# Optimization experiments

Hardware: AMD Instinct MI355X
Metric: run time of the kernel (lower is better)

Reference implementation:

```python
import jax, jax.numpy as jnp
import numpy as np

NUM_GROUPS = 16
EPS = 1e-6


def setup_inputs() -> dict:
    key = jax.random.key(0)
    ks = jax.random.split(key, 6)
    b, c, t, h, w = 2, 256, 4, 32, 32
    x = jax.random.normal(ks[0], (b, c, t, h, w), dtype=jnp.float32)
    scale = 0.02
    return {
        "x": x,
        "gamma": jnp.ones((c,), jnp.float32),
        "beta": jnp.zeros((c,), jnp.float32),
        "wq": jax.random.normal(ks[1], (c, c), jnp.float32) * scale,
        "bq": jnp.zeros((c,), jnp.float32),
        "wk": jax.random.normal(ks[2], (c, c), jnp.float32) * scale,
        "bk": jnp.zeros((c,), jnp.float32),
        "wv": jax.random.normal(ks[3], (c, c), jnp.float32) * scale,
        "bv": jnp.zeros((c,), jnp.float32),
        "wp": jax.random.normal(ks[4], (c, c), jnp.float32) * scale,
        "bp": jnp.zeros((c,), jnp.float32),
    }


def _group_norm(x, gamma, beta):
    b, c, t, h, w = x.shape
    xg = x.reshape(b, NUM_GROUPS, -1)  # [b, G, (c/G)*t*h*w]
    mu = jnp.mean(xg, axis=2, keepdims=True)
    var = jnp.var(xg, axis=2, keepdims=True)
    xn = ((xg - mu) * jax.lax.rsqrt(var + EPS)).reshape(b, c, t, h, w)
    return xn * gamma[None, :, None, None, None] + beta[None, :, None, None, None]


def reference(x, gamma, beta, wq, bq, wk, bk, wv, bv, wp, bp):
    b, c, t, h, w = x.shape
    n = t * h * w
    hn = _group_norm(x, gamma, beta).reshape(b, c, n)  # [b, c, n]
    # 1x1x1 conv == channel matmul
    q = jnp.einsum("oc,bcn->bon", wq, hn) + bq[None, :, None]
    k = jnp.einsum("oc,bcn->bon", wk, hn) + bk[None, :, None]
    v = jnp.einsum("oc,bcn->bon", wv, hn) + bv[None, :, None]
    # scores[b, i, j] = sum_c q[b,c,i] k[b,c,j] / sqrt(c)
    scores = jnp.einsum("bci,bcj->bij", q, k) * (float(c) ** -0.5)
    attn = jax.nn.softmax(scores, axis=2)  # [b, n, n]
    # h_[b, c, i] = sum_j v[b,c,j] attn[b,i,j]
    ho = jnp.einsum("bcj,bij->bci", v, attn)
    out = jnp.einsum("oc,bcn->bon", wp, ho) + bp[None, :, None]
    return x + out.reshape(b, c, t, h, w)
```

## Files before the change

kernel.cpp:

```cpp
#include <hip/hip_runtime.h>
#include <hip/hip_bf16.h>

#define NB 2
#define NC 256
#define NN 4096
#define NG 16
#define GSZ (16*NN)
#define SPLIT 4
#define JT (NN / SPLIT / 64)
#define SCL 0.09014205f
#define THRRAW 88.0f

typedef __attribute__((ext_vector_type(8))) short bf16x8;
typedef __attribute__((ext_vector_type(4))) float f32x4;
typedef __attribute__((ext_vector_type(8))) unsigned short u16x8;

static __device__ __forceinline__ unsigned short f2b(float f) {
    union { float f; unsigned u; } x; x.f = f;
    unsigned r = x.u + 0x7fffu + ((x.u >> 16) & 1u);
    return (unsigned short)(r >> 16);
}
static __device__ __forceinline__ float b2f(unsigned short u) {
    union { unsigned u; float f; } x; x.u = ((unsigned)u) << 16;
    return x.f;
}
static __device__ __forceinline__ void glds16(const void* g, void* l) {
    __builtin_amdgcn_global_load_lds(
        (const __attribute__((address_space(1))) unsigned int*)g,
        (__attribute__((address_space(3))) unsigned int*)l, 16, 0, 0);
}

__global__ void k_wcvt(const float* __restrict__ wq, const float* __restrict__ wk,
                       const float* __restrict__ wv, const float* __restrict__ wp,
                       unsigned short* __restrict__ dst) {
    int idx = (blockIdx.x * 256 + threadIdx.x) * 4;
    int which = idx >> 16, off = idx & 65535;
    const float* s = (which == 0) ? wq : (which == 1) ? wk : (which == 2) ? wv : wp;
    float4 v = *(const float4*)(s + off);
    dst[idx + 0] = f2b(v.x);
    dst[idx + 1] = f2b(v.y);
    dst[idx + 2] = f2b(v.z);
    dst[idx + 3] = f2b(v.w);
}

__global__ void k_stats(const float* __restrict__ x, float* __restrict__ stats) {
    int bg = blockIdx.x >> 3, seg = blockIdx.x & 7;
    const float4* p = (const float4*)(x + (size_t)bg * GSZ + (size_t)seg * (GSZ / 8));
    float s1 = 0.f, s2 = 0.f;
    for (int k = threadIdx.x; k < GSZ / 8 / 4; k += 256) {
        float4 v = p[k];
        s1 += v.x + v.y + v.z + v.w;
        s2 += v.x*v.x + v.y*v.y + v.z*v.z + v.w*v.w;
    }
    #pragma unroll
    for (int m = 1; m < 64; m <<= 1) { s1 += __shfl_xor(s1, m); s2 += __shfl_xor(s2, m); }
    __shared__ float r1[4], r2[4];
    int w = threadIdx.x >> 6;
    if ((threadIdx.x & 63) == 0) { r1[w] = s1; r2[w] = s2; }
    __syncthreads();
    if (threadIdx.x == 0) {
        float a = 0.f, b = 0.f;
        #pragma unroll
        for (int i = 0; i < 4; i++) { a += r1[i]; b += r2[i]; }
        atomicAdd(&stats[bg * 2], a);
        atomicAdd(&stats[bg * 2 + 1], b);
    }
}

__global__ void k_norm_t(const float* __restrict__ x, const float* __restrict__ gamma,
                         const float* __restrict__ beta, const float* __restrict__ stats,
                         unsigned short* __restrict__ hn_t) {
    __shared__ unsigned short tile[64][66];
    int n0 = blockIdx.x * 64, c0 = blockIdx.y * 64, b = blockIdx.z;
    int cc = threadIdx.x >> 2, part = threadIdx.x & 3;
    int c = c0 + cc;
    float s1 = stats[(b * NG + (c >> 4)) * 2];
    float s2 = stats[(b * NG + (c >> 4)) * 2 + 1];
    float mean = s1 * (1.f / (float)GSZ);
    float var  = s2 * (1.f / (float)GSZ) - mean * mean;
    float rstd = rsqrtf(var + 1e-6f);
    float sc = rstd * gamma[c];
    float sh = beta[c] - mean * sc;
    const float4* row = (const float4*)(x + ((size_t)b * NC + c) * NN + n0);
    #pragma unroll
    for (int q = 0; q < 4; q++) {
        int f4 = part * 4 + q;
        float4 v = row[f4];
        tile[cc][f4*4+0] = f2b(v.x * sc + sh);
        tile[cc][f4*4+1] = f2b(v.y * sc + sh);
        tile[cc][f4*4+2] = f2b(v.z * sc + sh);
        tile[cc][f4*4+3] = f2b(v.w * sc + sh);
    }
    __syncthreads();
    int nn = threadIdx.x >> 2;
    u16x8 o0, o1;
    #pragma unroll
    for (int e = 0; e < 8; e++) { o0[e] = tile[part*16 + e][nn]; o1[e] = tile[part*16 + 8 + e][nn]; }
    unsigned short* dst = hn_t + ((size_t)b * NN + n0 + nn) * NC + c0 + part * 16;
    *(u16x8*)dst = o0;
    *(u16x8*)(dst + 8) = o1;
}

__global__ __launch_bounds__(256, 2) void k_qkv(
        const unsigned short* __restrict__ hn_t, const unsigned short* __restrict__ wb,
        const float* __restrict__ bq, const float* __restrict__ bk, const float* __restrict__ bv,
        unsigned short* __restrict__ q_t, unsigned short* __restrict__ k_t,
        unsigned short* __restrict__ v_cm) {
    int i0 = blockIdx.x * 64, which = blockIdx.y, b = blockIdx.z;
    int lane = threadIdx.x & 63, w = threadIdx.x >> 6;
    const unsigned short* W = wb + which * 65536;
    const float* bias = (which == 0) ? bq : (which == 1) ? bk : bv;
    if (which < 2) {
        const unsigned short* arow =
            hn_t + ((size_t)b * NN + i0 + w * 16 + (lane & 15)) * NC + ((lane >> 4) * 8);
        f32x4 acc[16];
        #pragma unroll
        for (int t = 0; t < 16; t++) acc[t] = (f32x4){0.f, 0.f, 0.f, 0.f};
        #pragma unroll
        for (int kk = 0; kk < 8; kk++) {
            bf16x8 af = *(const bf16x8*)(arow + kk * 32);
            const unsigned short* bbase = W + (size_t)(lane & 15) * NC + kk * 32 + ((lane >> 4) * 8);
            #pragma unroll
            for (int ot = 0; ot < 16; ot++) {
                bf16x8 bf_ = *(const bf16x8*)(bbase + (size_t)ot * 16 * NC);
                acc[ot] = __builtin_amdgcn_mfma_f32_16x16x32_bf16(af, bf_, acc[ot], 0, 0, 0);
            }
        }
        unsigned short* dst = ((which == 0) ? q_t : k_t) + (size_t)b * NN * NC;
        #pragma unroll
        for (int ot = 0; ot < 16; ot++) {
            float bv_ = bias[ot * 16 + (lane & 15)];
            #pragma unroll
            for (int r = 0; r < 4; r++) {
                int i = i0 + w * 16 + (lane >> 4) * 4 + r;
                dst[(size_t)i * NC + ot * 16 + (lane & 15)] = f2b(acc[ot][r] + bv_);
            }
        }
    } else {
        f32x4 acc[4][4];
        #pragma unroll
        for (int mt = 0; mt < 4; mt++)
            #pragma unroll
            for (int nt = 0; nt < 4; nt++) acc[mt][nt] = (f32x4){0.f, 0.f, 0.f, 0.f};
        #pragma unroll
        for (int kk = 0; kk < 8; kk++) {
            bf16x8 bfr[4];
            #pragma unroll
            for (int nt = 0; nt < 4; nt++)
                bfr[nt] = *(const bf16x8*)(hn_t + ((size_t)b * NN + i0 + nt * 16 + (lane & 15)) * NC
                                           + kk * 32 + ((lane >> 4) * 8));
            #pragma unroll
            for (int mt = 0; mt < 4; mt++) {
                bf16x8 af = *(const bf16x8*)(W + (size_t)(w * 64 + mt * 16 + (lane & 15)) * NC
                                             + kk * 32 + ((lane >> 4) * 8));
                #pragma unroll
                for (int nt = 0; nt < 4; nt++)
                    acc[mt][nt] = __builtin_amdgcn_mfma_f32_16x16x32_bf16(af, bfr[nt], acc[mt][nt], 0, 0, 0);
            }
        }
        #pragma unroll
        for (int mt = 0; mt < 4; mt++) {
            #pragma unroll
            for (int r = 0; r < 4; r++) {
                int o = w * 64 + mt * 16 + (lane >> 4) * 4 + r;
                float bv_ = bias[o];
                #pragma unroll
                for (int nt = 0; nt < 4; nt++) {
                    int i = i0 + nt * 16 + (lane & 15);
                    v_cm[(size_t)b * NC * NN + (size_t)o * NN + i] = f2b(acc[mt][nt][r] + bv_);
                }
            }
        }
    }
}

__global__ __launch_bounds__(512, 2) void k_attn(
        const unsigned short* __restrict__ q_t, const unsigned short* __restrict__ k_t,
        const unsigned short* __restrict__ v_cm,
        unsigned short* __restrict__ po, float* __restrict__ ml) {
    __shared__ __attribute__((aligned(16))) unsigned short Ks[2][16384];
    __shared__ __attribute__((aligned(16))) unsigned short Vs[2][16384];
    __shared__ __attribute__((aligned(16))) unsigned short Ps[8][1024];
    int bid = blockIdx.x;
    int g = bid & 7, xb = bid >> 3;
    int sp = g & 3, b = g >> 2;
    int i0 = xb * 128;
    int lane = threadIdx.x & 63, w = threadIdx.x >> 6;
    size_t bO = (size_t)b * NN * NC;
    bf16x8 qf[8];
    {
        const unsigned short* qrow =
            q_t + bO + (size_t)(i0 + w * 16 + (lane & 15)) * NC + ((lane >> 4) * 8);
        #pragma unroll
        for (int kk = 0; kk < 8; kk++) qf[kk] = *(const bf16x8*)(qrow + kk * 32);
    }
    unsigned kstat[4], vstat[4];
    #pragma unroll
    for (int r = 0; r < 4; r++) {
        int jr = r * 16 + w * 2 + (lane >> 5);
        kstat[r] = (unsigned)(jr * 512 + (((lane & 31) * 16) ^ ((jr & 7) << 4)));
        int cr = r * 64 + w * 8 + (lane >> 3);
        vstat[r] = (unsigned)(cr * 8192 + (((lane & 7) * 16) ^ ((cr & 7) << 4)));
    }
    const char* kp = (const char*)(k_t + bO) + (size_t)sp * 524288;
    const char* vp = (const char*)(v_cm + bO) + (size_t)sp * 2048;
    f32x4 o[16];
    #pragma unroll
    for (int t = 0; t < 16; t++) o[t] = (f32x4){0.f, 0.f, 0.f, 0.f};
    float m = -1e30f, l = 0.f;
    #pragma unroll
    for (int r = 0; r < 4; r++) {
        glds16(kp + kstat[r], (char*)&Ks[0][0] + w * 1024 + r * 8192);
        glds16(vp + vstat[r], (char*)&Vs[0][0] + w * 1024 + r * 8192);
    }
    __syncthreads();
    int cur = 0;
    #pragma unroll 1
    for (int t = 0; t < JT; ++t) {
        if (t < JT - 1) {
            kp += 32768; vp += 128;
            int nb = cur ^ 1;
            #pragma unroll
            for (int r = 0; r < 4; r++) {
                glds16(kp + kstat[r], (char*)&Ks[nb][0] + w * 1024 + r * 8192);
                glds16(vp + vstat[r], (char*)&Vs[nb][0] + w * 1024 + r * 8192);
            }
        }
        const char* KsB = (const char*)&Ks[cur][0];
        const char* VsB = (const char*)&Vs[cur][0];
        f32x4 s[4];
        #pragma unroll
        for (int tt = 0; tt < 4; tt++) s[tt] = (f32x4){0.f, 0.f, 0.f, 0.f};
        __builtin_amdgcn_s_setprio(1);
        #pragma unroll
        for (int kk = 0; kk < 8; kk++) {
            #pragma unroll
            for (int tt = 0; tt < 4; tt++) {
                unsigned off = ((unsigned)((tt * 16 + (lane & 15)) * 512 + kk * 64 + ((lane >> 4) * 16)))
                               ^ (((unsigned)(lane & 7)) << 4);
                bf16x8 kf = *(const bf16x8*)(KsB + off);
                s[tt] = __builtin_amdgcn_mfma_f32_16x16x32_bf16(kf, qf[kk], s[tt], 0, 0, 0);
            }
        }
        __builtin_amdgcn_s_setprio(0);
        float lm = -1e30f;
        #pragma unroll
        for (int tt = 0; tt < 4; tt++)
            #pragma unroll
            for (int r = 0; r < 4; r++) lm = fmaxf(lm, s[tt][r]);
        lm = fmaxf(lm, __shfl_xor(lm, 16));
        lm = fmaxf(lm, __shfl_xor(lm, 32));
        float tmax = lm - m;
        tmax = fmaxf(tmax, __shfl_xor(tmax, 1));
        tmax = fmaxf(tmax, __shfl_xor(tmax, 2));
        tmax = fmaxf(tmax, __shfl_xor(tmax, 4));
        tmax = fmaxf(tmax, __shfl_xor(tmax, 8));
        if (tmax > THRRAW) {
            float mn = fmaxf(m, lm);
            float corr = exp2f((m - mn) * SCL);
            m = mn;
            l *= corr;
            #pragma unroll
            for (int r = 0; r < 4; r++) {
                float cr_ = __shfl(corr, (lane & 48) | ((lane >> 4) * 4 + r));
                #pragma unroll
                for (int ct = 0; ct < 16; ct++) o[ct][r] *= cr_;
            }
        }
        float rs = 0.f;
        #pragma unroll
        for (int tt = 0; tt < 4; tt++) {
            unsigned long long pw = 0ull;
            #pragma unroll
            for (int r = 0; r < 4; r++) {
                float p = exp2f((s[tt][r] - m) * SCL);
                rs += p;
                pw |= (unsigned long long)f2b(p) << (r * 16);
            }
            unsigned off = ((unsigned)((lane & 15) * 128 + tt * 32 + ((lane >> 4) * 8)))
                           ^ (((unsigned)(lane & 7)) << 4);
            *(unsigned long long*)((char*)&Ps[w][0] + off) = pw;
        }
        rs += __shfl_xor(rs, 16);
        rs += __shfl_xor(rs, 32);
        l += rs;
        __builtin_amdgcn_s_setprio(1);
        #pragma unroll
        for (int kk = 0; kk < 2; kk++) {
            unsigned offp = ((unsigned)((lane & 15) * 128 + kk * 64 + ((lane >> 4) * 16)))
                            ^ (((unsigned)(lane & 7)) << 4);
            bf16x8 pf = *(const bf16x8*)((char*)&Ps[w][0] + offp);
            #pragma unroll
            for (int ct = 0; ct < 16; ct++) {
                unsigned offv = ((unsigned)((ct * 16 + (lane & 15)) * 128 + kk * 64 + ((lane >> 4) * 16)))
                                ^ (((unsigned)(lane & 7)) << 4);
                bf16x8 vf = *(const bf16x8*)(VsB + offv);
                o[ct] = __builtin_amdgcn_mfma_f32_16x16x32_bf16(pf, vf, o[ct], 0, 0, 0);
            }
        }
        __builtin_amdgcn_s_setprio(0);
        __syncthreads();
        cur ^= 1;
    }
    unsigned short* dst = po + (size_t)(sp * NB + b) * NN * NC;
    #pragma unroll
    for (int ct = 0; ct < 16; ct++) {
        #pragma unroll
        for (int r = 0; r < 4; r++) {
            int i = i0 + w * 16 + (lane >> 4) * 4 + r;
            dst[(size_t)i * NC + ct * 16 + (lane & 15)] = f2b(o[ct][r]);
        }
    }
    if (lane < 16) {
        int i = i0 + w * 16 + lane;
        size_t mi = ((size_t)(sp * NB + b) * NN + i) * 2;
        ml[mi] = m;
        ml[mi + 1] = l;
    }
}

__global__ __launch_bounds__(256, 4) void k_proj(
        const unsigned short* __restrict__ po, const float* __restrict__ ml,
        const unsigned short* __restrict__ wp_b, const float* __restrict__ bp,
        const float* __restrict__ x, float* __restrict__ out) {
    __shared__ __attribute__((aligned(16))) unsigned short Hs[32 * 256];
    int i0 = blockIdx.x * 32, b = blockIdx.y;
    int tid = threadIdx.x, lane = tid & 63, w = tid >> 6;
    {
        int il = tid >> 3, cq = tid & 7;
        int i = i0 + il;
        float mv[SPLIT], lv[SPLIT];
        float M = -1e30f;
        #pragma unroll
        for (int s = 0; s < SPLIT; s++) {
            size_t mi = ((size_t)(s * NB + b) * NN + i) * 2;
            mv[s] = ml[mi]; lv[s] = ml[mi + 1];
            M = fmaxf(M, mv[s]);
        }
        float den = 0.f, wg[SPLIT];
        #pragma unroll
        for (int s = 0; s < SPLIT; s++) { wg[s] = exp2f((mv[s] - M) * SCL); den += wg[s] * lv[s]; }
        float inv = 1.f / den;
        #pragma unroll
        for (int s = 0; s < SPLIT; s++) wg[s] *= inv;
        #pragma unroll
        for (int e = 0; e < 4; e++) {
            float accv[8];
            #pragma unroll
            for (int q = 0; q < 8; q++) accv[q] = 0.f;
            #pragma unroll
            for (int s = 0; s < SPLIT; s++) {
                u16x8 v = *(const u16x8*)(po + ((size_t)(s * NB + b) * NN + i) * NC + cq * 32 + e * 8);
                #pragma unroll
                for (int q = 0; q < 8; q++) accv[q] += wg[s] * b2f(v[q]);
            }
            u16x8 rv;
            #pragma unroll
            for (int q = 0; q < 8; q++) rv[q] = f2b(accv[q]);
            unsigned off = ((unsigned)(il * 512 + cq * 64 + e * 16)) ^ ((il & 7) << 4);
            *(u16x8*)((char*)Hs + off) = rv;
        }
    }
    __syncthreads();
    f32x4 acc[4][2];
    #pragma unroll
    for (int mt = 0; mt < 4; mt++)
        #pragma unroll
        for (int nt = 0; nt < 2; nt++) acc[mt][nt] = (f32x4){0.f, 0.f, 0.f, 0.f};
    #pragma unroll
    for (int kk = 0; kk < 8; kk++) {
        bf16x8 bfr[2];
        #pragma unroll
        for (int nt = 0; nt < 2; nt++) {
            unsigned off = ((unsigned)((nt * 16 + (lane & 15)) * 512 + kk * 64 + ((lane >> 4) * 16)))
                           ^ (((unsigned)(lane & 7)) << 4);
            bfr[nt] = *(const bf16x8*)((char*)Hs + off);
        }
        #pragma unroll
        for (int mt = 0; mt < 4; mt++) {
            bf16x8 af = *(const bf16x8*)(wp_b + (size_t)(w * 64 + mt * 16 + (lane & 15)) * NC
                                         + kk * 32 + ((lane >> 4) * 8));
            #pragma unroll
            for (int nt = 0; nt < 2; nt++)
                acc[mt][nt] = __builtin_amdgcn_mfma_f32_16x16x32_bf16(af, bfr[nt], acc[mt][nt], 0, 0, 0);
        }
    }
    #pragma unroll
    for (int mt = 0; mt < 4; mt++) {
        #pragma unroll
        for (int r = 0; r < 4; r++) {
            int o = w * 64 + mt * 16 + (lane >> 4) * 4 + r;
            float bv_ = bp[o];
            #pragma unroll
            for (int nt = 0; nt < 2; nt++) {
                int i = i0 + nt * 16 + (lane & 15);
                size_t idx = ((size_t)b * NC + o) * NN + i;
                out[idx] = x[idx] + acc[mt][nt][r] + bv_;
            }
        }
    }
}

extern "C" void kernel_launch(void* const* d_in, const int* in_sizes, int n_in,
                              void* d_out, int out_size, void* d_ws, size_t ws_size,
                              hipStream_t stream) {
    const float* x     = (const float*)d_in[0];
    const float* gamma = (const float*)d_in[1];
    const float* beta  = (const float*)d_in[2];
    const float* wq    = (const float*)d_in[3];
    const float* bq    = (const float*)d_in[4];
    const float* wk    = (const float*)d_in[5];
    const float* bk    = (const float*)d_in[6];
    const float* wv    = (const float*)d_in[7];
    const float* bv    = (const float*)d_in[8];
    const float* wp    = (const float*)d_in[9];
    const float* bp    = (const float*)d_in[10];
    float* out = (float*)d_out;

    char* ws = (char*)d_ws;
    const size_t MB = 1024 * 1024;
    float*          stats = (float*)ws;
    unsigned short* wb    = (unsigned short*)(ws + 1024);
    unsigned short* q_t   = (unsigned short*)(ws + 1 * MB);
    unsigned short* k_t   = (unsigned short*)(ws + 5 * MB);
    unsigned short* v_cm  = (unsigned short*)(ws + 9 * MB);
    float*          ml    = (float*)(ws + 13 * MB);
    unsigned short* hn_t  = (unsigned short*)(ws + 14 * MB);
    unsigned short* po    = (unsigned short*)(ws + 14 * MB);

    hipMemsetAsync(stats, 0, 1024, stream);
    k_wcvt<<<256, 256, 0, stream>>>(wq, wk, wv, wp, wb);
    k_stats<<<256, 256, 0, stream>>>(x, stats);
    k_norm_t<<<dim3(NN / 64, NC / 64, NB), 256, 0, stream>>>(x, gamma, beta, stats, hn_t);
    k_qkv<<<dim3(NN / 64, 3, NB), 256, 0, stream>>>(hn_t, wb, bq, bk, bv, q_t, k_t, v_cm);
    k_attn<<<256, 512, 0, stream>>>(q_t, k_t, v_cm, po, ml);
    k_proj<<<dim3(NN / 32, NB), 256, 0, stream>>>(po, ml, wb + 3 * 65536, bp, x, out);
}
```

Measured before the change: 203.3 us.

## Fuse group-norm apply into QKV projection and merge stats with weight conversion

Weight conversion and group-norm statistics now run in one launch, selected by block index. The normalize-and-transpose kernel is removed. Each QKV block normalizes a 32-column slice of x into swizzled LDS, then computes Q, K and V from it. This drops two launches and the round trip of the bf16 hn_t buffer through global memory, at the cost of smaller per-block tiles and weight reads repeated across more blocks.

```diff
diff --git a/kernel.cpp b/kernel.cpp
--- a/kernel.cpp
+++ b/kernel.cpp
@@ -30,131 +30,142 @@
         (__attribute__((address_space(3))) unsigned int*)l, 16, 0, 0);
 }
 
-__global__ void k_wcvt(const float* __restrict__ wq, const float* __restrict__ wk,
-                       const float* __restrict__ wv, const float* __restrict__ wp,
-                       unsigned short* __restrict__ dst) {
-    int idx = (blockIdx.x * 256 + threadIdx.x) * 4;
-    int which = idx >> 16, off = idx & 65535;
-    const float* s = (which == 0) ? wq : (which == 1) ? wk : (which == 2) ? wv : wp;
-    float4 v = *(const float4*)(s + off);
-    dst[idx + 0] = f2b(v.x);
-    dst[idx + 1] = f2b(v.y);
-    dst[idx + 2] = f2b(v.z);
-    dst[idx + 3] = f2b(v.w);
-}
-
-__global__ void k_stats(const float* __restrict__ x, float* __restrict__ stats) {
-    int bg = blockIdx.x >> 3, seg = blockIdx.x & 7;
-    const float4* p = (const float4*)(x + (size_t)bg * GSZ + (size_t)seg * (GSZ / 8));
-    float s1 = 0.f, s2 = 0.f;
-    for (int k = threadIdx.x; k < GSZ / 8 / 4; k += 256) {
-        float4 v = p[k];
-        s1 += v.x + v.y + v.z + v.w;
-        s2 += v.x*v.x + v.y*v.y + v.z*v.z + v.w*v.w;
-    }
-    #pragma unroll
-    for (int m = 1; m < 64; m <<= 1) { s1 += __shfl_xor(s1, m); s2 += __shfl_xor(s2, m); }
+__global__ void k_pre(const float* __restrict__ wq, const float* __restrict__ wk,
+                      const float* __restrict__ wv, const float* __restrict__ wp,
+                      unsigned short* __restrict__ wbd,
+                      const float* __restrict__ x, float* __restrict__ stats) {
     __shared__ float r1[4], r2[4];
-    int w = threadIdx.x >> 6;
-    if ((threadIdx.x & 63) == 0) { r1[w] = s1; r2[w] = s2; }
-    __syncthreads();
-    if (threadIdx.x == 0) {
-        float a = 0.f, b = 0.f;
-        #pragma unroll
-        for (int i = 0; i < 4; i++) { a += r1[i]; b += r2[i]; }
-        atomicAdd(&stats[bg * 2], a);
-        atomicAdd(&stats[bg * 2 + 1], b);
-    }
-}
-
-__global__ void k_norm_t(const float* __restrict__ x, const float* __restrict__ gamma,
-                         const float* __restrict__ beta, const float* __restrict__ stats,
-                         unsigned short* __restrict__ hn_t) {
-    __shared__ unsigned short tile[64][66];
-    int n0 = blockIdx.x * 64, c0 = blockIdx.y * 64, b = blockIdx.z;
-    int cc = threadIdx.x >> 2, part = threadIdx.x & 3;
-    int c = c0 + cc;
-    float s1 = stats[(b * NG + (c >> 4)) * 2];
-    float s2 = stats[(b * NG + (c >> 4)) * 2 + 1];
-    float mean = s1 * (1.f / (float)GSZ);
-    float var  = s2 * (1.f / (float)GSZ) - mean * mean;
-    float rstd = rsqrtf(var + 1e-6f);
-    float sc = rstd * gamma[c];
-    float sh = beta[c] - mean * sc;
-    const float4* row = (const float4*)(x + ((size_t)b * NC + c) * NN + n0);
-    #pragma unroll
-    for (int q = 0; q < 4; q++) {
-        int f4 = part * 4 + q;
-        float4 v = row[f4];
-        tile[cc][f4*4+0] = f2b(v.x * sc + sh);
-        tile[cc][f4*4+1] = f2b(v.y * sc + sh);
-        tile[cc][f4*4+2] = f2b(v.z * sc + sh);
-        tile[cc][f4*4+3] = f2b(v.w * sc + sh);
-    }
-    __syncthreads();
-    int nn = threadIdx.x >> 2;
-    u16x8 o0, o1;
-    #pragma unroll
-    for (int e = 0; e < 8; e++) { o0[e] = tile[part*16 + e][nn]; o1[e] = tile[part*16 + 8 + e][nn]; }
-    unsigned short* dst = hn_t + ((size_t)b * NN + n0 + nn) * NC + c0 + part * 16;
-    *(u16x8*)dst = o0;
-    *(u16x8*)(dst + 8) = o1;
-}
-
-__global__ __launch_bounds__(256, 2) void k_qkv(
-        const unsigned short* __restrict__ hn_t, const unsigned short* __restrict__ wb,
+    int bx = blockIdx.x;
+    if (bx < 256) {
+        int bg = bx >> 3, seg = bx & 7;
+        const float4* p = (const float4*)(x + (size_t)bg * GSZ + (size_t)seg * (GSZ / 8));
+        float s1 = 0.f, s2 = 0.f;
+        for (int k = threadIdx.x; k < GSZ / 8 / 4; k += 256) {
+            float4 v = p[k];
+            s1 += v.x + v.y + v.z + v.w;
+            s2 += v.x*v.x + v.y*v.y + v.z*v.z + v.w*v.w;
+        }
+        #pragma unroll
+        for (int m = 1; m < 64; m <<= 1) { s1 += __shfl_xor(s1, m); s2 += __shfl_xor(s2, m); }
+        int w = threadIdx.x >> 6;
+        if ((threadIdx.x & 63) == 0) { r1[w] = s1; r2[w] = s2; }
+        __syncthreads();
+        if (threadIdx.x == 0) {
+            float a = 0.f, b = 0.f;
+            #pragma unroll
+            for (int i = 0; i < 4; i++) { a += r1[i]; b += r2[i]; }
+            atomicAdd(&stats[bg * 2], a);
+            atomicAdd(&stats[bg * 2 + 1], b);
+        }
+    } else {
+        int idx = ((bx - 256) * 256 + threadIdx.x) * 4;
+        int which = idx >> 16, off = idx & 65535;
+        const float* s = (which == 0) ? wq : (which == 1) ? wk : (which == 2) ? wv : wp;
+        float4 v = *(const float4*)(s + off);
+        wbd[idx + 0] = f2b(v.x);
+        wbd[idx + 1] = f2b(v.y);
+        wbd[idx + 2] = f2b(v.z);
+        wbd[idx + 3] = f2b(v.w);
+    }
+}
+
+__global__ __launch_bounds__(256, 2) void k_qkvn(
+        const float* __restrict__ x, const float* __restrict__ gamma,
+        const float* __restrict__ beta, const float* __restrict__ stats,
+        const unsigned short* __restrict__ wb,
         const float* __restrict__ bq, const float* __restrict__ bk, const float* __restrict__ bv,
         unsigned short* __restrict__ q_t, unsigned short* __restrict__ k_t,
         unsigned short* __restrict__ v_cm) {
-    int i0 = blockIdx.x * 64, which = blockIdx.y, b = blockIdx.z;
-    int lane = threadIdx.x & 63, w = threadIdx.x >> 6;
-    const unsigned short* W = wb + which * 65536;
-    const float* bias = (which == 0) ? bq : (which == 1) ? bk : bv;
-    if (which < 2) {
-        const unsigned short* arow =
-            hn_t + ((size_t)b * NN + i0 + w * 16 + (lane & 15)) * NC + ((lane >> 4) * 8);
-        f32x4 acc[16];
-        #pragma unroll
-        for (int t = 0; t < 16; t++) acc[t] = (f32x4){0.f, 0.f, 0.f, 0.f};
+    __shared__ __attribute__((aligned(16))) unsigned short hs[32 * 256];
+    int i0 = blockIdx.x * 32, b = blockIdx.y;
+    int tid = threadIdx.x, lane = tid & 63, w = tid >> 6;
+    {
+        int c = tid;
+        float s1 = stats[(b * NG + (c >> 4)) * 2];
+        float s2 = stats[(b * NG + (c >> 4)) * 2 + 1];
+        float mean = s1 * (1.f / (float)GSZ);
+        float var  = s2 * (1.f / (float)GSZ) - mean * mean;
+        float rstd = rsqrtf(var + 1e-6f);
+        float sc = rstd * gamma[c];
+        float sh = beta[c] - mean * sc;
+        const float4* row = (const float4*)(x + ((size_t)b * NC + c) * NN + i0);
+        #pragma unroll
+        for (int q = 0; q < 8; q++) {
+            float4 v = row[q];
+            float vals[4] = {v.x, v.y, v.z, v.w};
+            #pragma unroll
+            for (int e = 0; e < 4; e++) {
+                int i = q * 4 + e;
+                unsigned off = (unsigned)(i * 512 + ((c * 2) ^ ((i & 7) << 4)));
+                *(unsigned short*)((char*)hs + off) = f2b(vals[e] * sc + sh);
+            }
+        }
+    }
+    __syncthreads();
+    #pragma unroll 1
+    for (int which = 0; which < 2; ++which) {
+        const unsigned short* W = wb + which * 65536;
+        const float* bias = (which == 0) ? bq : bk;
+        unsigned short* dst = ((which == 0) ? q_t : k_t) + (size_t)b * NN * NC;
+        f32x4 acc[2][4];
+        #pragma unroll
+        for (int it = 0; it < 2; it++)
+            #pragma unroll
+            for (int ot = 0; ot < 4; ot++) acc[it][ot] = (f32x4){0.f, 0.f, 0.f, 0.f};
         #pragma unroll
         for (int kk = 0; kk < 8; kk++) {
-            bf16x8 af = *(const bf16x8*)(arow + kk * 32);
-            const unsigned short* bbase = W + (size_t)(lane & 15) * NC + kk * 32 + ((lane >> 4) * 8);
-            #pragma unroll
-            for (int ot = 0; ot < 16; ot++) {
-                bf16x8 bf_ = *(const bf16x8*)(bbase + (size_t)ot * 16 * NC);
-                acc[ot] = __builtin_amdgcn_mfma_f32_16x16x32_bf16(af, bf_, acc[ot], 0, 0, 0);
-            }
-        }
-        unsigned short* dst = ((which == 0) ? q_t : k_t) + (size_t)b * NN * NC;
-        #pragma unroll
-        for (int ot = 0; ot < 16; ot++) {
-            float bv_ = bias[ot * 16 + (lane & 15)];
-            #pragma unroll
-            for (int r = 0; r < 4; r++) {
-                int i = i0 + w * 16 + (lane >> 4) * 4 + r;
-                dst[(size_t)i * NC + ot * 16 + (lane & 15)] = f2b(acc[ot][r] + bv_);
-            }
-        }
-    } else {
-        f32x4 acc[4][4];
+            bf16x8 af[2];
+            #pragma unroll
+            for (int it = 0; it < 2; it++) {
+                unsigned row = (unsigned)(it * 16 + (lane & 15));
+                unsigned off = row * 512 + (((unsigned)(kk * 64 + ((lane >> 4) * 16))) ^ ((row & 7) << 4));
+                af[it] = *(const bf16x8*)((char*)hs + off);
+            }
+            #pragma unroll
+            for (int ot = 0; ot < 4; ot++) {
+                bf16x8 bf_ = *(const bf16x8*)(W + (size_t)(w * 64 + ot * 16 + (lane & 15)) * NC
+                                              + kk * 32 + ((lane >> 4) * 8));
+                #pragma unroll
+                for (int it = 0; it < 2; it++)
+                    acc[it][ot] = __builtin_amdgcn_mfma_f32_16x16x32_bf16(af[it], bf_, acc[it][ot], 0, 0, 0);
+            }
+        }
+        #pragma unroll
+        for (int it = 0; it < 2; it++) {
+            #pragma unroll
+            for (int ot = 0; ot < 4; ot++) {
+                int o = w * 64 + ot * 16 + (lane & 15);
+                float bv_ = bias[o];
+                #pragma unroll
+                for (int r = 0; r < 4; r++) {
+                    int i = i0 + it * 16 + (lane >> 4) * 4 + r;
+                    dst[(size_t)i * NC + o] = f2b(acc[it][ot][r] + bv_);
+                }
+            }
+        }
+    }
+    {
+        const unsigned short* W = wb + 2 * 65536;
+        f32x4 acc[4][2];
         #pragma unroll
         for (int mt = 0; mt < 4; mt++)
             #pragma unroll
-            for (int nt = 0; nt < 4; nt++) acc[mt][nt] = (f32x4){0.f, 0.f, 0.f, 0.f};
+            for (int nt = 0; nt < 2; nt++) acc[mt][nt] = (f32x4){0.f, 0.f, 0.f, 0.f};
         #pragma unroll
         for (int kk = 0; kk < 8; kk++) {
-            bf16x8 bfr[4];
-            #pragma unroll
-            for (int nt = 0; nt < 4; nt++)
-                bfr[nt] = *(const bf16x8*)(hn_t + ((size_t)b * NN + i0 + nt * 16 + (lane & 15)) * NC
-                                           + kk * 32 + ((lane >> 4) * 8));
+            bf16x8 bfr[2];
+            #pragma unroll
+            for (int nt = 0; nt < 2; nt++) {
+                unsigned row = (unsigned)(nt * 16 + (lane & 15));
+                unsigned off = row * 512 + (((unsigned)(kk * 64 + ((lane >> 4) * 16))) ^ ((row & 7) << 4));
+                bfr[nt] = *(const bf16x8*)((char*)hs + off);
+            }
             #pragma unroll
             for (int mt = 0; mt < 4; mt++) {
                 bf16x8 af = *(const bf16x8*)(W + (size_t)(w * 64 + mt * 16 + (lane & 15)) * NC
                                              + kk * 32 + ((lane >> 4) * 8));
                 #pragma unroll
-                for (int nt = 0; nt < 4; nt++)
+                for (int nt = 0; nt < 2; nt++)
                     acc[mt][nt] = __builtin_amdgcn_mfma_f32_16x16x32_bf16(af, bfr[nt], acc[mt][nt], 0, 0, 0);
             }
         }
@@ -163,9 +174,9 @@
             #pragma unroll
             for (int r = 0; r < 4; r++) {
                 int o = w * 64 + mt * 16 + (lane >> 4) * 4 + r;
-                float bv_ = bias[o];
-                #pragma unroll
-                for (int nt = 0; nt < 4; nt++) {
+                float bv_ = bv[o];
+                #pragma unroll
+                for (int nt = 0; nt < 2; nt++) {
                     int i = i0 + nt * 16 + (lane & 15);
                     v_cm[(size_t)b * NC * NN + (size_t)o * NN + i] = f2b(acc[mt][nt][r] + bv_);
                 }
@@ -425,14 +436,12 @@
     unsigned short* k_t   = (unsigned short*)(ws + 5 * MB);
     unsigned short* v_cm  = (unsigned short*)(ws + 9 * MB);
     float*          ml    = (float*)(ws + 13 * MB);
-    unsigned short* hn_t  = (unsigned short*)(ws + 14 * MB);
     unsigned short* po    = (unsigned short*)(ws + 14 * MB);
 
     hipMemsetAsync(stats, 0, 1024, stream);
-    k_wcvt<<<256, 256, 0, stream>>>(wq, wk, wv, wp, wb);
-    k_stats<<<256, 256, 0, stream>>>(x, stats);
-    k_norm_t<<<dim3(NN / 64, NC / 64, NB), 256, 0, stream>>>(x, gamma, beta, stats, hn_t);
-    k_qkv<<<dim3(NN / 64, 3, NB), 256, 0, stream>>>(hn_t, wb, bq, bk, bv, q_t, k_t, v_cm);
+    k_pre<<<512, 256, 0, stream>>>(wq, wk, wv, wp, wb, x, stats);
+    k_qkvn<<<dim3(NN / 32, NB), 256, 0, stream>>>(x, gamma, beta, stats, wb,
+                                                  bq, bk, bv, q_t, k_t, v_cm);
     k_attn<<<256, 512, 0, stream>>>(q_t, k_t, v_cm, po, ml);
     k_proj<<<dim3(NN / 32, NB), 256, 0, stream>>>(po, ml, wb + 3 * 65536, bp, x, out);
 }
```

After: 186.5 us. 1.09x faster.
